# Kernel optimization log

Hardware: AMD Instinct MI355X
Metric: run time of the kernel (lower is better)

The kernel has to match this reference:

```python
import jax, jax.numpy as jnp
import numpy as np

N_NODES = 50000
N_EDGES = 800000
NFEAT = 128
NHID = 128
NCLASS = 10
NUM_GRAPHS = 512


def setup_inputs() -> dict:
    key = jax.random.key(0)
    ks = jax.random.split(key, 8)
    node_feat = jax.random.normal(ks[0], (N_NODES, NFEAT), dtype=jnp.float32)
    W1 = jax.random.normal(ks[1], (NFEAT, NHID), dtype=jnp.float32) * (1.0 / np.sqrt(NFEAT))
    W2 = jax.random.normal(ks[2], (NHID, NHID), dtype=jnp.float32) * (1.0 / np.sqrt(NHID))
    mlp_w = jax.random.normal(ks[3], (NHID, NCLASS), dtype=jnp.float32) * (1.0 / np.sqrt(NHID))
    mlp_b = jnp.zeros((NCLASS,), dtype=jnp.float32)
    edge_src = jax.random.randint(ks[4], (N_EDGES,), 0, N_NODES, dtype=jnp.int32)
    edge_dst = jax.random.randint(ks[5], (N_EDGES,), 0, N_NODES, dtype=jnp.int32)
    graph_ids = jnp.sort(jax.random.randint(ks[6], (N_NODES,), 0, NUM_GRAPHS, dtype=jnp.int32))
    return {"node_feat": node_feat, "W1": W1, "W2": W2, "mlp_w": mlp_w,
            "mlp_b": mlp_b, "edge_src": edge_src, "edge_dst": edge_dst,
            "graph_ids": graph_ids}


def reference(node_feat, W1, W2, mlp_w, mlp_b, edge_src, edge_dst, graph_ids):
    # node_degs: in-degree + 1 (self loop), as used by GraphConvolution's normalization
    ones_e = jnp.ones((N_EDGES,), dtype=node_feat.dtype)
    deg = jax.ops.segment_sum(ones_e, edge_dst, num_segments=N_NODES) + 1.0  # [N]

    def gconv(x, W):
        h = x @ W                                                     # [N, H]
        msg = jax.ops.segment_sum(h[edge_src], edge_dst, num_segments=N_NODES)
        return (h + msg) / deg[:, None]                               # mean over self + neighbors

    x = jax.nn.relu(gconv(node_feat, W1))
    x = gconv(x, W2)                                                  # [N, NHID]

    # per-graph mean readout (the Python loop over graph_sizes == segment mean)
    counts = jax.ops.segment_sum(jnp.ones((N_NODES,), x.dtype), graph_ids,
                                 num_segments=NUM_GRAPHS)             # [G]
    gsum = jax.ops.segment_sum(x, graph_ids, num_segments=NUM_GRAPHS)  # [G, NHID]
    gmean = gsum / jnp.maximum(counts, 1.0)[:, None]

    logits = gmean @ mlp_w + mlp_b                                    # [G, NCLASS]
    return jax.nn.log_softmax(logits, axis=1)
```

## Files before the change

kernel.cpp:

```cpp
#include <hip/hip_runtime.h>

#define N_NODES 50000
#define N_EDGES 800000
#define NFEAT 128
#define NHID 128
#define NCLASS 10
#define NUM_GRAPHS 512
#define GEMM_BLOCKS 782
#define SLOT 64

#define G1_GEMM 782
#define G1_BKT 1024
#define G1_GRID (G1_GEMM + G1_BKT)

typedef __attribute__((ext_vector_type(8))) short bf16x8;
typedef __attribute__((ext_vector_type(4))) float f32x4;

__device__ inline ushort f2bf(float f) {
  union { float f; uint u; } c; c.f = f;
  return (ushort)((c.u + 0x7fffu + ((c.u >> 16) & 1u)) >> 16);
}
__device__ inline float bf2f_lo(uint u) { union { uint u; float f; } c; c.u = u << 16; return c.f; }
__device__ inline float bf2f_hi(uint u) { union { uint u; float f; } c; c.u = u & 0xffff0000u; return c.f; }
__device__ inline float bf2f_s(ushort h) { union { uint u; float f; } c; c.u = ((uint)h) << 16; return c.f; }

template <bool XFP32>
__device__ inline void gemm_body(const void* __restrict__ Xv,
                                 const ushort* __restrict__ Wp,
                                 ushort* __restrict__ Y,
                                 ushort* xs, ushort* wsh,
                                 int base, int tid) {
  const int rem = N_NODES - base;
  for (int i = tid; i < 2048; i += 256)
    ((uint4*)wsh)[i] = ((const uint4*)Wp)[i];

  for (int g = tid; g < 1024; g += 256) {
    int row = g >> 4;
    int k0 = (g & 15) << 3;
    int wt = row >> 4, ks = k0 >> 5;
    int lane = (row & 15) + (((k0 >> 3) & 3) << 4);
    uint4 v;
    if (row < rem) {
      if (XFP32) {
        const float* s = (const float*)Xv + (size_t)(base + row) * 128 + k0;
        float4 p0 = ((const float4*)s)[0];
        float4 p1 = ((const float4*)s)[1];
        v.x = (uint)f2bf(p0.x) | ((uint)f2bf(p0.y) << 16);
        v.y = (uint)f2bf(p0.z) | ((uint)f2bf(p0.w) << 16);
        v.z = (uint)f2bf(p1.x) | ((uint)f2bf(p1.y) << 16);
        v.w = (uint)f2bf(p1.z) | ((uint)f2bf(p1.w) << 16);
      } else {
        v = *(const uint4*)((const ushort*)Xv + (size_t)(base + row) * 128 + k0);
      }
    } else {
      v.x = 0; v.y = 0; v.z = 0; v.w = 0;
    }
    *(uint4*)&xs[((((wt << 2) + ks) << 6) + lane) << 3] = v;
  }
  __syncthreads();

  const int wave = tid >> 6, lane = tid & 63;
  f32x4 acc[8];
#pragma unroll
  for (int i = 0; i < 8; ++i) acc[i] = f32x4{0.f, 0.f, 0.f, 0.f};
  bf16x8 a[4];
#pragma unroll
  for (int ks = 0; ks < 4; ++ks)
    a[ks] = *(const bf16x8*)&xs[((((wave << 2) + ks) << 6) + lane) << 3];
#pragma unroll
  for (int ks = 0; ks < 4; ++ks) {
#pragma unroll
    for (int nt = 0; nt < 8; ++nt) {
      bf16x8 b = *(const bf16x8*)&wsh[((((nt << 2) + ks) << 6) + lane) << 3];
      acc[nt] = __builtin_amdgcn_mfma_f32_16x16x32_bf16(a[ks], b, acc[nt], 0, 0, 0);
    }
  }
  const int r0 = base + wave * 16 + ((lane >> 4) << 2);
  const int c0 = lane & 15;
#pragma unroll
  for (int nt = 0; nt < 8; ++nt)
#pragma unroll
    for (int r = 0; r < 4; ++r) {
      int row = r0 + r;
      if (row < N_NODES)
        Y[(size_t)row * 128 + (nt << 4) + c0] = f2bf(acc[nt][r]);
    }
}

__global__ __launch_bounds__(256) void k_wpack(const float* __restrict__ W1,
                                               const float* __restrict__ W2,
                                               ushort* __restrict__ wp1,
                                               ushort* __restrict__ wp2) {
  int idx = blockIdx.x * 256 + threadIdx.x;
  const float* W = (idx < 16384) ? W1 : W2;
  ushort* op = (idx < 16384) ? wp1 : wp2;
  int j = idx & 16383;
  int lane = (j >> 3) & 63;
  int e = j & 7;
  int frag = j >> 9;
  int nt = frag >> 2, ks = frag & 3;
  int c = nt * 16 + (lane & 15);
  int k = ks * 32 + (lane >> 4) * 8 + e;
  op[j] = f2bf(W[k * 128 + c]);
}

__global__ __launch_bounds__(256) void k_fused1(const float* __restrict__ feat,
                                                const ushort* __restrict__ wp1,
                                                const int* __restrict__ esrc,
                                                const int* __restrict__ edst,
                                                int* __restrict__ cnt,
                                                ushort* __restrict__ csr16,
                                                ushort* __restrict__ Y) {
  __shared__ ushort xs[4 * 4 * 64 * 8];
  __shared__ ushort wsh[32 * 64 * 8];
  const int b = blockIdx.x;
  const int tid = threadIdx.x;
  if (b < G1_GEMM) {
    gemm_body<true>(feat, wp1, Y, xs, wsh, b * 64, tid);
  } else {
    for (int e = (b - G1_GEMM) * 256 + tid; e < N_EDGES; e += G1_BKT * 256) {
      int d = edst[e];
      int p = atomicAdd(&cnt[d], 1);
      if (p < SLOT) csr16[(size_t)d * SLOT + p] = (ushort)esrc[e];
    }
  }
}

__global__ __launch_bounds__(256) void k_agg1(const ushort* __restrict__ H,
                                              const ushort* __restrict__ csr16,
                                              const int* __restrict__ cnt,
                                              ushort* __restrict__ Out) {
  const int node = blockIdx.x * 4 + (threadIdx.x >> 6);
  const int lane = threadIdx.x & 63;
  const int deg = min(cnt[node], SLOT);
  const ushort* nb = csr16 + (size_t)node * SLOT;
  const uint* __restrict__ H2 = (const uint*)H;
  float ax = 0.f, ay = 0.f;
  int e = 0;
  for (; e + 8 <= deg; e += 8) {
    uint4 iv = *(const uint4*)(nb + e);
    uint s0 = iv.x & 0xffffu, s1 = iv.x >> 16, s2 = iv.y & 0xffffu, s3 = iv.y >> 16;
    uint s4 = iv.z & 0xffffu, s5 = iv.z >> 16, s6 = iv.w & 0xffffu, s7 = iv.w >> 16;
    uint u0 = H2[(size_t)s0 * 64 + lane];
    uint u1 = H2[(size_t)s1 * 64 + lane];
    uint u2 = H2[(size_t)s2 * 64 + lane];
    uint u3 = H2[(size_t)s3 * 64 + lane];
    uint u4 = H2[(size_t)s4 * 64 + lane];
    uint u5 = H2[(size_t)s5 * 64 + lane];
    uint u6 = H2[(size_t)s6 * 64 + lane];
    uint u7 = H2[(size_t)s7 * 64 + lane];
    ax += ((bf2f_lo(u0) + bf2f_lo(u1)) + (bf2f_lo(u2) + bf2f_lo(u3))) +
          ((bf2f_lo(u4) + bf2f_lo(u5)) + (bf2f_lo(u6) + bf2f_lo(u7)));
    ay += ((bf2f_hi(u0) + bf2f_hi(u1)) + (bf2f_hi(u2) + bf2f_hi(u3))) +
          ((bf2f_hi(u4) + bf2f_hi(u5)) + (bf2f_hi(u6) + bf2f_hi(u7)));
  }
  if (e + 4 <= deg) {
    uint2 iv = *(const uint2*)(nb + e);
    uint s0 = iv.x & 0xffffu, s1 = iv.x >> 16, s2 = iv.y & 0xffffu, s3 = iv.y >> 16;
    uint u0 = H2[(size_t)s0 * 64 + lane];
    uint u1 = H2[(size_t)s1 * 64 + lane];
    uint u2 = H2[(size_t)s2 * 64 + lane];
    uint u3 = H2[(size_t)s3 * 64 + lane];
    ax += (bf2f_lo(u0) + bf2f_lo(u1)) + (bf2f_lo(u2) + bf2f_lo(u3));
    ay += (bf2f_hi(u0) + bf2f_hi(u1)) + (bf2f_hi(u2) + bf2f_hi(u3));
    e += 4;
  }
  for (; e < deg; ++e) {
    uint u = H2[(size_t)nb[e] * 64 + lane];
    ax += bf2f_lo(u);
    ay += bf2f_hi(u);
  }
  uint uh = H2[(size_t)node * 64 + lane];
  float inv = 1.0f / (float)(deg + 1);
  float rx = fmaxf((bf2f_lo(uh) + ax) * inv, 0.f);
  float ry = fmaxf((bf2f_hi(uh) + ay) * inv, 0.f);
  ((uint*)Out)[(size_t)node * 64 + lane] = (uint)f2bf(rx) | ((uint)f2bf(ry) << 16);
}

__global__ __launch_bounds__(256) void k_gemm2(const ushort* __restrict__ X,
                                               const ushort* __restrict__ Wp,
                                               ushort* __restrict__ Y) {
  __shared__ ushort xs[4 * 4 * 64 * 8];
  __shared__ ushort wsh[32 * 64 * 8];
  gemm_body<false>(X, Wp, Y, xs, wsh, blockIdx.x * 64, threadIdx.x);
}

__global__ __launch_bounds__(256) void k_agg_ro(const ushort* __restrict__ H,
                                                const ushort* __restrict__ csr16,
                                                const int* __restrict__ cnt,
                                                const int* __restrict__ gid,
                                                float* __restrict__ gsum,
                                                float* __restrict__ gcnt) {
  __shared__ float rows[4][128];
  __shared__ int gids[4];
  const int w = threadIdx.x >> 6;
  const int lane = threadIdx.x & 63;
  const int node = blockIdx.x * 4 + w;
  const int deg = min(cnt[node], SLOT);
  const ushort* nb = csr16 + (size_t)node * SLOT;
  const uint* __restrict__ H2 = (const uint*)H;
  float ax = 0.f, ay = 0.f;
  int e = 0;
  for (; e + 8 <= deg; e += 8) {
    uint4 iv = *(const uint4*)(nb + e);
    uint s0 = iv.x & 0xffffu, s1 = iv.x >> 16, s2 = iv.y & 0xffffu, s3 = iv.y >> 16;
    uint s4 = iv.z & 0xffffu, s5 = iv.z >> 16, s6 = iv.w & 0xffffu, s7 = iv.w >> 16;
    uint u0 = H2[(size_t)s0 * 64 + lane];
    uint u1 = H2[(size_t)s1 * 64 + lane];
    uint u2 = H2[(size_t)s2 * 64 + lane];
    uint u3 = H2[(size_t)s3 * 64 + lane];
    uint u4 = H2[(size_t)s4 * 64 + lane];
    uint u5 = H2[(size_t)s5 * 64 + lane];
    uint u6 = H2[(size_t)s6 * 64 + lane];
    uint u7 = H2[(size_t)s7 * 64 + lane];
    ax += ((bf2f_lo(u0) + bf2f_lo(u1)) + (bf2f_lo(u2) + bf2f_lo(u3))) +
          ((bf2f_lo(u4) + bf2f_lo(u5)) + (bf2f_lo(u6) + bf2f_lo(u7)));
    ay += ((bf2f_hi(u0) + bf2f_hi(u1)) + (bf2f_hi(u2) + bf2f_hi(u3))) +
          ((bf2f_hi(u4) + bf2f_hi(u5)) + (bf2f_hi(u6) + bf2f_hi(u7)));
  }
  if (e + 4 <= deg) {
    uint2 iv = *(const uint2*)(nb + e);
    uint s0 = iv.x & 0xffffu, s1 = iv.x >> 16, s2 = iv.y & 0xffffu, s3 = iv.y >> 16;
    uint u0 = H2[(size_t)s0 * 64 + lane];
    uint u1 = H2[(size_t)s1 * 64 + lane];
    uint u2 = H2[(size_t)s2 * 64 + lane];
    uint u3 = H2[(size_t)s3 * 64 + lane];
    ax += (bf2f_lo(u0) + bf2f_lo(u1)) + (bf2f_lo(u2) + bf2f_lo(u3));
    ay += (bf2f_hi(u0) + bf2f_hi(u1)) + (bf2f_hi(u2) + bf2f_hi(u3));
    e += 4;
  }
  for (; e < deg; ++e) {
    uint u = H2[(size_t)nb[e] * 64 + lane];
    ax += bf2f_lo(u);
    ay += bf2f_hi(u);
  }
  uint uh = H2[(size_t)node * 64 + lane];
  float inv = 1.0f / (float)(deg + 1);
  float rx = bf2f_s(f2bf((bf2f_lo(uh) + ax) * inv));
  float ry = bf2f_s(f2bf((bf2f_hi(uh) + ay) * inv));
  *(float2*)&rows[w][lane * 2] = make_float2(rx, ry);
  if (lane == 0) gids[w] = gid[node];
  __syncthreads();
  const int t = threadIdx.x;
  if (t < 128) {
    float acc = rows[0][t];
    int g = gids[0];
#pragma unroll
    for (int r = 1; r < 4; ++r) {
      int gr = gids[r];
      if (gr != g) {
        atomicAdd(&gsum[g * 128 + t], acc);
        acc = 0.f;
        g = gr;
      }
      acc += rows[r][t];
    }
    atomicAdd(&gsum[g * 128 + t], acc);
  } else if (t == 128) {
    float c = 1.f;
    int g = gids[0];
#pragma unroll
    for (int r = 1; r < 4; ++r) {
      int gr = gids[r];
      if (gr != g) {
        atomicAdd(&gcnt[g], c);
        c = 0.f;
        g = gr;
      }
      c += 1.f;
    }
    atomicAdd(&gcnt[g], c);
  }
}

__global__ __launch_bounds__(128) void k_mlp(const float* __restrict__ gsum,
                                             const float* __restrict__ gcnt,
                                             const float* __restrict__ Wm,
                                             const float* __restrict__ bm,
                                             float* __restrict__ out) {
  __shared__ float m[128];
  __shared__ float lg[NCLASS];
  const int g = blockIdx.x;
  const int t = threadIdx.x;
  float cnt = fmaxf(gcnt[g], 1.0f);
  m[t] = gsum[g * 128 + t] / cnt;
  __syncthreads();
  if (t < NCLASS) {
    float s = bm[t];
#pragma unroll
    for (int k = 0; k < 128; ++k) s += m[k] * Wm[k * NCLASS + t];
    lg[t] = s;
  }
  __syncthreads();
  if (t < NCLASS) {
    float mx = lg[0];
#pragma unroll
    for (int i = 1; i < NCLASS; ++i) mx = fmaxf(mx, lg[i]);
    float sum = 0.f;
#pragma unroll
    for (int i = 0; i < NCLASS; ++i) sum += expf(lg[i] - mx);
    out[g * NCLASS + t] = lg[t] - mx - logf(sum);
  }
}

extern "C" void kernel_launch(void* const* d_in, const int* in_sizes, int n_in,
                              void* d_out, int out_size, void* d_ws, size_t ws_size,
                              hipStream_t stream) {
  const float* feat = (const float*)d_in[0];
  const float* W1   = (const float*)d_in[1];
  const float* W2   = (const float*)d_in[2];
  const float* Wm   = (const float*)d_in[3];
  const float* bm   = (const float*)d_in[4];
  const int* esrc   = (const int*)d_in[5];
  const int* edst   = (const int*)d_in[6];
  const int* gid    = (const int*)d_in[7];
  float* out = (float*)d_out;

  int* cnt      = (int*)d_ws;
  ushort* csr16 = (ushort*)(cnt + 50048);
  ushort* wp1   = csr16 + (size_t)N_NODES * SLOT;
  ushort* wp2   = wp1 + 16384;
  ushort* bufA  = wp2 + 16384;
  ushort* bufB  = bufA + (size_t)N_NODES * NHID;
  float* gsum   = (float*)(bufB + (size_t)N_NODES * NHID);
  float* gcnt   = gsum + NUM_GRAPHS * NHID;

  hipMemsetAsync(cnt, 0, (size_t)50048 * sizeof(int), stream);
  hipMemsetAsync(gsum, 0, (size_t)(NUM_GRAPHS * NHID + 512) * sizeof(float), stream);

  k_wpack<<<128, 256, 0, stream>>>(W1, W2, wp1, wp2);

  k_fused1<<<G1_GRID, 256, 0, stream>>>(feat, wp1, esrc, edst, cnt, csr16, bufA);

  k_agg1<<<N_NODES / 4, 256, 0, stream>>>(bufA, csr16, cnt, bufB);

  k_gemm2<<<GEMM_BLOCKS, 256, 0, stream>>>(bufB, wp2, bufA);

  k_agg_ro<<<N_NODES / 4, 256, 0, stream>>>(bufA, csr16, cnt, gid, gsum, gcnt);

  k_mlp<<<NUM_GRAPHS, 128, 0, stream>>>(gsum, gcnt, Wm, bm, out);
}
```

Baseline: 261.4 us.

## Partition CSR build by destination slice and gather two nodes per wave

The edge-bucketing blocks are split into 8 groups, each scanning all edges but only inserting those whose destination falls into its node slice, to localize atomics and CSR writes (likely per XCD). The aggregation kernels now process two nodes per wavefront with 8-byte loads per lane, and the readout reduces 8 rows per block before global atomics. The trade-off is 8x re-reading of the edge destination array in exchange for better locality and fewer, wider gather instructions.

Result: faster. 232.1 us (-11.2%).

```diff
diff --git a/kernel.cpp b/kernel.cpp
--- a/kernel.cpp
+++ b/kernel.cpp
@@ -8,6 +8,7 @@
 #define NUM_GRAPHS 512
 #define GEMM_BLOCKS 782
 #define SLOT 64
+#define NSLICE 6250
 
 #define G1_GEMM 782
 #define G1_BKT 1024
@@ -118,63 +119,80 @@
   if (b < G1_GEMM) {
     gemm_body<true>(feat, wp1, Y, xs, wsh, b * 64, tid);
   } else {
-    for (int e = (b - G1_GEMM) * 256 + tid; e < N_EDGES; e += G1_BKT * 256) {
+    const int g = b & 7;
+    const int m = (b - G1_GEMM) >> 3;
+    const int lo = g * NSLICE, hi = lo + NSLICE;
+    for (int e = m * 256 + tid; e < N_EDGES; e += 128 * 256) {
       int d = edst[e];
-      int p = atomicAdd(&cnt[d], 1);
-      if (p < SLOT) csr16[(size_t)d * SLOT + p] = (ushort)esrc[e];
-    }
-  }
+      if (d >= lo && d < hi) {
+        int p = atomicAdd(&cnt[d], 1);
+        if (p < SLOT) csr16[(size_t)d * SLOT + p] = (ushort)esrc[e];
+      }
+    }
+  }
+}
+
+__device__ inline void unpack_add(uint2 u, float4& a) {
+  a.x += bf2f_lo(u.x); a.y += bf2f_hi(u.x);
+  a.z += bf2f_lo(u.y); a.w += bf2f_hi(u.y);
+}
+
+__device__ inline float4 gather_sum(const uint2* __restrict__ Hv,
+                                    const ushort* __restrict__ nb,
+                                    int deg, int q) {
+  float4 a = {0.f, 0.f, 0.f, 0.f};
+  int e = 0;
+  for (; e + 8 <= deg; e += 8) {
+    uint4 iv = *(const uint4*)(nb + e);
+    uint2 u0 = Hv[(size_t)(iv.x & 0xffffu) * 32 + q];
+    uint2 u1 = Hv[(size_t)(iv.x >> 16) * 32 + q];
+    uint2 u2 = Hv[(size_t)(iv.y & 0xffffu) * 32 + q];
+    uint2 u3 = Hv[(size_t)(iv.y >> 16) * 32 + q];
+    uint2 u4 = Hv[(size_t)(iv.z & 0xffffu) * 32 + q];
+    uint2 u5 = Hv[(size_t)(iv.z >> 16) * 32 + q];
+    uint2 u6 = Hv[(size_t)(iv.w & 0xffffu) * 32 + q];
+    uint2 u7 = Hv[(size_t)(iv.w >> 16) * 32 + q];
+    unpack_add(u0, a); unpack_add(u1, a); unpack_add(u2, a); unpack_add(u3, a);
+    unpack_add(u4, a); unpack_add(u5, a); unpack_add(u6, a); unpack_add(u7, a);
+  }
+  if (e + 4 <= deg) {
+    uint2 iv = *(const uint2*)(nb + e);
+    uint2 u0 = Hv[(size_t)(iv.x & 0xffffu) * 32 + q];
+    uint2 u1 = Hv[(size_t)(iv.x >> 16) * 32 + q];
+    uint2 u2 = Hv[(size_t)(iv.y & 0xffffu) * 32 + q];
+    uint2 u3 = Hv[(size_t)(iv.y >> 16) * 32 + q];
+    unpack_add(u0, a); unpack_add(u1, a); unpack_add(u2, a); unpack_add(u3, a);
+    e += 4;
+  }
+  for (; e < deg; ++e) {
+    uint2 u = Hv[(size_t)nb[e] * 32 + q];
+    unpack_add(u, a);
+  }
+  return a;
 }
 
 __global__ __launch_bounds__(256) void k_agg1(const ushort* __restrict__ H,
                                               const ushort* __restrict__ csr16,
                                               const int* __restrict__ cnt,
                                               ushort* __restrict__ Out) {
-  const int node = blockIdx.x * 4 + (threadIdx.x >> 6);
-  const int lane = threadIdx.x & 63;
+  const int w = threadIdx.x >> 6;
+  const int l = threadIdx.x & 63;
+  const int h = l >> 5, q = l & 31;
+  const int node = blockIdx.x * 8 + w * 2 + h;
   const int deg = min(cnt[node], SLOT);
   const ushort* nb = csr16 + (size_t)node * SLOT;
-  const uint* __restrict__ H2 = (const uint*)H;
-  float ax = 0.f, ay = 0.f;
-  int e = 0;
-  for (; e + 8 <= deg; e += 8) {
-    uint4 iv = *(const uint4*)(nb + e);
-    uint s0 = iv.x & 0xffffu, s1 = iv.x >> 16, s2 = iv.y & 0xffffu, s3 = iv.y >> 16;
-    uint s4 = iv.z & 0xffffu, s5 = iv.z >> 16, s6 = iv.w & 0xffffu, s7 = iv.w >> 16;
-    uint u0 = H2[(size_t)s0 * 64 + lane];
-    uint u1 = H2[(size_t)s1 * 64 + lane];
-    uint u2 = H2[(size_t)s2 * 64 + lane];
-    uint u3 = H2[(size_t)s3 * 64 + lane];
-    uint u4 = H2[(size_t)s4 * 64 + lane];
-    uint u5 = H2[(size_t)s5 * 64 + lane];
-    uint u6 = H2[(size_t)s6 * 64 + lane];
-    uint u7 = H2[(size_t)s7 * 64 + lane];
-    ax += ((bf2f_lo(u0) + bf2f_lo(u1)) + (bf2f_lo(u2) + bf2f_lo(u3))) +
-          ((bf2f_lo(u4) + bf2f_lo(u5)) + (bf2f_lo(u6) + bf2f_lo(u7)));
-    ay += ((bf2f_hi(u0) + bf2f_hi(u1)) + (bf2f_hi(u2) + bf2f_hi(u3))) +
-          ((bf2f_hi(u4) + bf2f_hi(u5)) + (bf2f_hi(u6) + bf2f_hi(u7)));
-  }
-  if (e + 4 <= deg) {
-    uint2 iv = *(const uint2*)(nb + e);
-    uint s0 = iv.x & 0xffffu, s1 = iv.x >> 16, s2 = iv.y & 0xffffu, s3 = iv.y >> 16;
-    uint u0 = H2[(size_t)s0 * 64 + lane];
-    uint u1 = H2[(size_t)s1 * 64 + lane];
-    uint u2 = H2[(size_t)s2 * 64 + lane];
-    uint u3 = H2[(size_t)s3 * 64 + lane];
-    ax += (bf2f_lo(u0) + bf2f_lo(u1)) + (bf2f_lo(u2) + bf2f_lo(u3));
-    ay += (bf2f_hi(u0) + bf2f_hi(u1)) + (bf2f_hi(u2) + bf2f_hi(u3));
-    e += 4;
-  }
-  for (; e < deg; ++e) {
-    uint u = H2[(size_t)nb[e] * 64 + lane];
-    ax += bf2f_lo(u);
-    ay += bf2f_hi(u);
-  }
-  uint uh = H2[(size_t)node * 64 + lane];
+  const uint2* __restrict__ Hv = (const uint2*)H;
+  float4 a = gather_sum(Hv, nb, deg, q);
+  uint2 uh = Hv[(size_t)node * 32 + q];
   float inv = 1.0f / (float)(deg + 1);
-  float rx = fmaxf((bf2f_lo(uh) + ax) * inv, 0.f);
-  float ry = fmaxf((bf2f_hi(uh) + ay) * inv, 0.f);
-  ((uint*)Out)[(size_t)node * 64 + lane] = (uint)f2bf(rx) | ((uint)f2bf(ry) << 16);
+  float r0 = fmaxf((bf2f_lo(uh.x) + a.x) * inv, 0.f);
+  float r1 = fmaxf((bf2f_hi(uh.x) + a.y) * inv, 0.f);
+  float r2 = fmaxf((bf2f_lo(uh.y) + a.z) * inv, 0.f);
+  float r3 = fmaxf((bf2f_hi(uh.y) + a.w) * inv, 0.f);
+  uint2 ov;
+  ov.x = (uint)f2bf(r0) | ((uint)f2bf(r1) << 16);
+  ov.y = (uint)f2bf(r2) | ((uint)f2bf(r3) << 16);
+  ((uint2*)Out)[(size_t)node * 32 + q] = ov;
 }
 
 __global__ __launch_bounds__(256) void k_gemm2(const ushort* __restrict__ X,
@@ -191,62 +209,33 @@
                                                 const int* __restrict__ gid,
                                                 float* __restrict__ gsum,
                                                 float* __restrict__ gcnt) {
-  __shared__ float rows[4][128];
-  __shared__ int gids[4];
+  __shared__ float rows[8][128];
+  __shared__ int gids[8];
   const int w = threadIdx.x >> 6;
-  const int lane = threadIdx.x & 63;
-  const int node = blockIdx.x * 4 + w;
+  const int l = threadIdx.x & 63;
+  const int h = l >> 5, q = l & 31;
+  const int slot = w * 2 + h;
+  const int node = blockIdx.x * 8 + slot;
   const int deg = min(cnt[node], SLOT);
   const ushort* nb = csr16 + (size_t)node * SLOT;
-  const uint* __restrict__ H2 = (const uint*)H;
-  float ax = 0.f, ay = 0.f;
-  int e = 0;
-  for (; e + 8 <= deg; e += 8) {
-    uint4 iv = *(const uint4*)(nb + e);
-    uint s0 = iv.x & 0xffffu, s1 = iv.x >> 16, s2 = iv.y & 0xffffu, s3 = iv.y >> 16;
-    uint s4 = iv.z & 0xffffu, s5 = iv.z >> 16, s6 = iv.w & 0xffffu, s7 = iv.w >> 16;
-    uint u0 = H2[(size_t)s0 * 64 + lane];
-    uint u1 = H2[(size_t)s1 * 64 + lane];
-    uint u2 = H2[(size_t)s2 * 64 + lane];
-    uint u3 = H2[(size_t)s3 * 64 + lane];
-    uint u4 = H2[(size_t)s4 * 64 + lane];
-    uint u5 = H2[(size_t)s5 * 64 + lane];
-    uint u6 = H2[(size_t)s6 * 64 + lane];
-    uint u7 = H2[(size_t)s7 * 64 + lane];
-    ax += ((bf2f_lo(u0) + bf2f_lo(u1)) + (bf2f_lo(u2) + bf2f_lo(u3))) +
-          ((bf2f_lo(u4) + bf2f_lo(u5)) + (bf2f_lo(u6) + bf2f_lo(u7)));
-    ay += ((bf2f_hi(u0) + bf2f_hi(u1)) + (bf2f_hi(u2) + bf2f_hi(u3))) +
-          ((bf2f_hi(u4) + bf2f_hi(u5)) + (bf2f_hi(u6) + bf2f_hi(u7)));
-  }
-  if (e + 4 <= deg) {
-    uint2 iv = *(const uint2*)(nb + e);
-    uint s0 = iv.x & 0xffffu, s1 = iv.x >> 16, s2 = iv.y & 0xffffu, s3 = iv.y >> 16;
-    uint u0 = H2[(size_t)s0 * 64 + lane];
-    uint u1 = H2[(size_t)s1 * 64 + lane];
-    uint u2 = H2[(size_t)s2 * 64 + lane];
-    uint u3 = H2[(size_t)s3 * 64 + lane];
-    ax += (bf2f_lo(u0) + bf2f_lo(u1)) + (bf2f_lo(u2) + bf2f_lo(u3));
-    ay += (bf2f_hi(u0) + bf2f_hi(u1)) + (bf2f_hi(u2) + bf2f_hi(u3));
-    e += 4;
-  }
-  for (; e < deg; ++e) {
-    uint u = H2[(size_t)nb[e] * 64 + lane];
-    ax += bf2f_lo(u);
-    ay += bf2f_hi(u);
-  }
-  uint uh = H2[(size_t)node * 64 + lane];
+  const uint2* __restrict__ Hv = (const uint2*)H;
+  float4 a = gather_sum(Hv, nb, deg, q);
+  uint2 uh = Hv[(size_t)node * 32 + q];
   float inv = 1.0f / (float)(deg + 1);
-  float rx = bf2f_s(f2bf((bf2f_lo(uh) + ax) * inv));
-  float ry = bf2f_s(f2bf((bf2f_hi(uh) + ay) * inv));
-  *(float2*)&rows[w][lane * 2] = make_float2(rx, ry);
-  if (lane == 0) gids[w] = gid[node];
+  float4 rr;
+  rr.x = bf2f_s(f2bf((bf2f_lo(uh.x) + a.x) * inv));
+  rr.y = bf2f_s(f2bf((bf2f_hi(uh.x) + a.y) * inv));
+  rr.z = bf2f_s(f2bf((bf2f_lo(uh.y) + a.z) * inv));
+  rr.w = bf2f_s(f2bf((bf2f_hi(uh.y) + a.w) * inv));
+  *(float4*)&rows[slot][q * 4] = rr;
+  if (q == 0) gids[slot] = gid[node];
   __syncthreads();
   const int t = threadIdx.x;
   if (t < 128) {
     float acc = rows[0][t];
     int g = gids[0];
 #pragma unroll
-    for (int r = 1; r < 4; ++r) {
+    for (int r = 1; r < 8; ++r) {
       int gr = gids[r];
       if (gr != g) {
         atomicAdd(&gsum[g * 128 + t], acc);
@@ -260,7 +249,7 @@
     float c = 1.f;
     int g = gids[0];
 #pragma unroll
-    for (int r = 1; r < 4; ++r) {
+    for (int r = 1; r < 8; ++r) {
       int gr = gids[r];
       if (gr != g) {
         atomicAdd(&gcnt[g], c);
@@ -332,11 +321,11 @@
 
   k_fused1<<<G1_GRID, 256, 0, stream>>>(feat, wp1, esrc, edst, cnt, csr16, bufA);
 
-  k_agg1<<<N_NODES / 4, 256, 0, stream>>>(bufA, csr16, cnt, bufB);
+  k_agg1<<<N_NODES / 8, 256, 0, stream>>>(bufA, csr16, cnt, bufB);
 
   k_gemm2<<<GEMM_BLOCKS, 256, 0, stream>>>(bufB, wp2, bufA);
 
-  k_agg_ro<<<N_NODES / 4, 256, 0, stream>>>(bufA, csr16, cnt, gid, gsum, gcnt);
+  k_agg_ro<<<N_NODES / 8, 256, 0, stream>>>(bufA, csr16, cnt, gid, gsum, gcnt);
 
   k_mlp<<<NUM_GRAPHS, 128, 0, stream>>>(gsum, gcnt, Wm, bm, out);
 }
```
